# Performance work log

Hardware: AMD Instinct MI355X
Metric: run time of the kernel (lower is better)

Reference implementation:

```python
import jax, jax.numpy as jnp
import numpy as np

N_ATOMS = 5000
N_EDGES = 100000
F = 128          # num_features
B = 20           # num_basis (sinc expansion)
L = 3            # num_interactions
CUTOFF = 5.0
NUM_EMB = 119


def setup_inputs() -> dict:
    key = jax.random.key(0)
    ks = jax.random.split(key, 16)
    Z = jax.random.randint(ks[0], (N_ATOMS,), 1, NUM_EMB)
    edge_idx = jax.random.randint(ks[1], (N_EDGES, 2), 0, N_ATOMS)
    edge_dist = jax.random.uniform(ks[2], (N_EDGES,), minval=0.5, maxval=6.0, dtype=jnp.float32)
    u = jax.random.normal(ks[3], (N_EDGES, 3), dtype=jnp.float32)
    u = u / jnp.linalg.norm(u, axis=-1, keepdims=True)
    edge_diff = u * edge_dist[:, None]  # displacement vectors with |d| == edge_dist
    s = lambda k, shape: (jax.random.normal(k, shape, dtype=jnp.float32) * 0.05)
    inp = dict(Z=Z, edge_idx=edge_idx, edge_diff=edge_diff, edge_dist=edge_dist)
    inp.update(
        emb=s(ks[4], (NUM_EMB, F)),
        msg_w1=s(ks[5], (L, F, F)), msg_b1=jnp.zeros((L, F), jnp.float32),
        msg_w2=s(ks[6], (L, F, 3 * F)), msg_b2=jnp.zeros((L, 3 * F), jnp.float32),
        filt_w=s(ks[7], (L, B, 3 * F)), filt_b=jnp.zeros((L, 3 * F), jnp.float32),
        upd_U=s(ks[8], (L, F, F)), upd_V=s(ks[9], (L, F, F)),
        upd_w1=s(ks[10], (L, 2 * F, F)), upd_b1=jnp.zeros((L, F), jnp.float32),
        upd_w2=s(ks[11], (L, F, 3 * F)), upd_b2=jnp.zeros((L, 3 * F), jnp.float32),
        ro_w1=s(ks[12], (F, F // 2)), ro_b1=jnp.zeros((F // 2,), jnp.float32),
        ro_w2=s(ks[13], (F // 2, 1)), ro_b2=jnp.zeros((1,), jnp.float32),
    )
    return inp


def _painn(Z, edge_idx, edge_diff, edge_dist,
           emb, msg_w1, msg_b1, msg_w2, msg_b2, filt_w, filt_b,
           upd_U, upd_V, upd_w1, upd_b1, upd_w2, upd_b2,
           ro_w1, ro_b1, ro_w2, ro_b2):
    dtype = edge_diff.dtype
    # edge mask (equivalent to boolean compaction: masked edges contribute 0)
    mask = (edge_dist < CUTOFF).astype(dtype)
    dst = edge_idx[:, 0]  # receiver (index_add target)
    src = edge_idx[:, 1]  # sender (gathered neighbor)
    # sinc radial expansion: sin(n*pi*r/rc)/r, n = 1..B
    n = jnp.arange(1, B + 1, dtype=dtype)
    rbf = jnp.sin(edge_dist[:, None] * n * (jnp.pi / CUTOFF)) / edge_dist[:, None]  # [E,B]
    # cosine cutoff envelope, zeroed outside cutoff
    fc = 0.5 * (jnp.cos(jnp.pi * edge_dist / CUTOFF) + 1.0)
    env = (fc * mask)[:, None]  # [E,1]
    unit = edge_diff / edge_dist[:, None]  # [E,3]

    s_feat = emb[Z]                                   # [N,F]
    v_feat = jnp.zeros((Z.shape[0], 3, F), dtype)     # [N,3,F]

    for l in range(L):
        # ---- PainnMessage ----
        filt = (rbf @ filt_w[l] + filt_b[l]) * env                           # [E,3F]
        phi = jax.nn.silu(s_feat @ msg_w1[l] + msg_b1[l]) @ msg_w2[l] + msg_b2[l]  # [N,3F]
        fo = filt * phi[src]                                                  # [E,3F]
        gsv, gev, ms = jnp.split(fo, 3, axis=-1)                              # each [E,F]
        mv = v_feat[src] * gsv[:, None, :] + gev[:, None, :] * unit[:, :, None]  # [E,3,F]
        s_feat = s_feat + jnp.zeros_like(s_feat).at[dst].add(ms)
        v_feat = v_feat + jnp.zeros_like(v_feat).at[dst].add(mv)
        # ---- PainnUpdate ----
        Uv = jnp.einsum('nif,fg->nig', v_feat, upd_U[l])   # [N,3,F]
        Vv = jnp.einsum('nif,fg->nig', v_feat, upd_V[l])   # [N,3,F]
        Vn = jnp.linalg.norm(Vv, axis=1)                   # [N,F]
        a = jax.nn.silu(jnp.concatenate([s_feat, Vn], axis=-1) @ upd_w1[l] + upd_b1[l]) @ upd_w2[l] + upd_b2[l]
        avv, asv, ass = jnp.split(a, 3, axis=-1)
        v_feat = v_feat + avv[:, None, :] * Uv
        s_feat = s_feat + asv * jnp.sum(Uv * Vv, axis=1) + ass

    # atomwise readout MLP -> per-atom energy
    atom_energy = (jax.nn.silu(s_feat @ ro_w1 + ro_b1) @ ro_w2 + ro_b2)[:, 0]  # [N]
    return atom_energy


def reference(Z, edge_idx, edge_diff, edge_dist,
              emb, msg_w1, msg_b1, msg_w2, msg_b2, filt_w, filt_b,
              upd_U, upd_V, upd_w1, upd_b1, upd_w2, upd_b2,
              ro_w1, ro_b1, ro_w2, ro_b2):
    return _painn(Z, edge_idx, edge_diff, edge_dist,
                  emb, msg_w1, msg_b1, msg_w2, msg_b2, filt_w, filt_b,
                  upd_U, upd_V, upd_w1, upd_b1, upd_w2, upd_b2,
                  ro_w1, ro_b1, ro_w2, ro_b2)
```

## Files before the change

kernel.cpp:

```cpp
#include <hip/hip_runtime.h>
#include <hip/hip_bf16.h>
#include <hip/hip_fp16.h>
#include <math.h>

#define N_ATOMS 5000
#define N_EDGES 100000
#define F 128
#define B 20
#define NL 3
#define CAP 64

constexpr float CUTOFF = 5.0f;
constexpr float PI_F = 3.14159265358979323846f;

typedef _Float16 f16x8 __attribute__((ext_vector_type(8)));
typedef _Float16 h2 __attribute__((ext_vector_type(2)));
typedef float f32x4 __attribute__((ext_vector_type(4)));

struct EMeta { int src; float env; float u0, u1, u2; int pad[3]; };
struct __align__(4) U3 { unsigned int x, y, z; };

__device__ __forceinline__ float silu_f(float x) { return x / (1.0f + __expf(-x)); }

#define PV_IDX(atom, t) (((size_t)(atom) * F + (t)) * 6)

__global__ void init_kernel(const int* __restrict__ Z, const float* __restrict__ emb,
                            float* __restrict__ s, _Float16* __restrict__ s_h,
                            float* __restrict__ v, _Float16* __restrict__ pv,
                            int* __restrict__ count) {
    int atom = blockIdx.x;
    int t = threadIdx.x;
    float val = emb[Z[atom] * F + t];
    s[atom * F + t] = val;
    s_h[atom * F + t] = (_Float16)val;
#pragma unroll
    for (int d = 0; d < 3; ++d) v[(size_t)atom * 3 * F + d * F + t] = 0.0f;
    unsigned int* pp = (unsigned int*)(pv + PV_IDX(atom, t));
    pp[0] = 0u; pp[1] = 0u; pp[2] = 0u;
    if (t == 0) count[atom] = 0;
}

__global__ void fill_buckets(const int* __restrict__ eidx, int* __restrict__ count,
                             int* __restrict__ bucket) {
    int e = blockIdx.x * 256 + threadIdx.x;
    if (e >= N_EDGES) return;
    int dst = eidx[2 * e];
    int pos = atomicAdd(&count[dst], 1);
    if (pos < CAP) bucket[dst * CAP + pos] = e;
}

__global__ void edge_meta_kernel(const int* __restrict__ count, const int* __restrict__ bucket,
                                 const int* __restrict__ eidx, const float* __restrict__ ediff,
                                 const float* __restrict__ edist,
                                 EMeta* __restrict__ meta, _Float16* __restrict__ rbfh) {
    int slot = blockIdx.x * 256 + threadIdx.x;
    if (slot >= N_ATOMS * CAP) return;
    int a = slot / CAP, i = slot % CAP;
    if (i >= count[a]) return;
    int e = bucket[slot];
    float d = edist[e];
    EMeta m;
    m.src = eidx[2 * e + 1];
    float fc = 0.5f * (cosf(PI_F * d / CUTOFF) + 1.0f);
    m.env = (d < CUTOFF) ? fc : 0.0f;
    float inv = 1.0f / d;
    m.u0 = ediff[3 * e + 0] * inv;
    m.u1 = ediff[3 * e + 1] * inv;
    m.u2 = ediff[3 * e + 2] * inv;
    m.pad[0] = m.pad[1] = m.pad[2] = 0;
    meta[slot] = m;
    _Float16* rp = rbfh + (size_t)slot * 24;
#pragma unroll
    for (int b = 0; b < B; ++b)
        rp[b] = (_Float16)(sinf(d * (float)(b + 1) * (PI_F / CUTOFF)) / d);
    rp[20] = rp[21] = rp[22] = rp[23] = (_Float16)0.0f;
}

struct TPlanX { const float* src; void* dst; int R, C, blk0, isf16, pad; };
struct TPlansX { TPlanX p[24]; int n; };

__global__ void transpose_x(TPlansX P) {
    int b = blockIdx.x;
    int pi = 0;
#pragma unroll
    for (int i = 1; i < 24; ++i)
        if (i < P.n && b >= P.p[i].blk0) pi = i;
    const float* src = P.p[pi].src;
    int R = P.p[pi].R, C = P.p[pi].C, pad = P.p[pi].pad;
    int f = (b - P.p[pi].blk0) * 256 + threadIdx.x;
    if (f < R * C) {
        int c = f / R, r = f - c * R;
        float val = src[r * C + c];
        if (P.p[pi].isf16) ((_Float16*)P.p[pi].dst)[c * pad + r] = (_Float16)val;
        else ((float*)P.p[pi].dst)[c * pad + r] = val;
    }
}

__global__ __launch_bounds__(256) void phi_mlp_kernel(
    const _Float16* __restrict__ s_h, const _Float16* __restrict__ w1T,
    const float* __restrict__ b1, const _Float16* __restrict__ w2T,
    const float* __restrict__ b2, _Float16* __restrict__ pv) {
    __shared__ __align__(16) _Float16 shA[16 * 136];
    __shared__ __align__(16) _Float16 shH[16 * 136];
    int r0 = blockIdx.x * 16;
    int tid = threadIdx.x;
    {
        int r = tid >> 4, c8 = (tid & 15) * 8;
        int rg = r0 + r; if (rg >= N_ATOMS) rg = N_ATOMS - 1;
        *(f16x8*)(shA + r * 136 + c8) = *(const f16x8*)(s_h + (size_t)rg * F + c8);
    }
    __syncthreads();
    int lane = tid & 63, wv = tid >> 6;
    int col = lane & 15, quad = lane >> 4;
    for (int nt = wv; nt < 8; nt += 4) {
        int n = nt * 16 + col;
        f32x4 acc = {0.f, 0.f, 0.f, 0.f};
#pragma unroll
        for (int kt = 0; kt < 4; ++kt) {
            f16x8 afr = *(const f16x8*)(shA + col * 136 + kt * 32 + quad * 8);
            f16x8 bfr = *(const f16x8*)(w1T + (size_t)n * 128 + kt * 32 + quad * 8);
            acc = __builtin_amdgcn_mfma_f32_16x16x32_f16(afr, bfr, acc, 0, 0, 0);
        }
        float bb = b1[n];
#pragma unroll
        for (int r = 0; r < 4; ++r)
            shH[(quad * 4 + r) * 136 + n] = (_Float16)silu_f(acc[r] + bb);
    }
    __syncthreads();
    for (int nt = wv; nt < 24; nt += 4) {
        int n = nt * 16 + col;
        f32x4 acc = {0.f, 0.f, 0.f, 0.f};
#pragma unroll
        for (int kt = 0; kt < 4; ++kt) {
            f16x8 afr = *(const f16x8*)(shH + col * 136 + kt * 32 + quad * 8);
            f16x8 bfr = *(const f16x8*)(w2T + (size_t)n * 128 + kt * 32 + quad * 8);
            acc = __builtin_amdgcn_mfma_f32_16x16x32_f16(afr, bfr, acc, 0, 0, 0);
        }
        float bb = b2[n];
#pragma unroll
        for (int r = 0; r < 4; ++r) {
            int row = r0 + quad * 4 + r;
            if (row < N_ATOMS)
                pv[PV_IDX(row, n & 127) + (n >> 7)] = (_Float16)(acc[r] + bb);
        }
    }
}

__global__ __launch_bounds__(256) void edge_agg_kernel(
    const int* __restrict__ count, const EMeta* __restrict__ meta,
    const _Float16* __restrict__ rbfh,
    const _Float16* __restrict__ fwT,
    const float* __restrict__ fb,
    const _Float16* __restrict__ pv,
    float* __restrict__ s, float* __restrict__ v,
    _Float16* __restrict__ vmid_h) {
    int a = blockIdx.x;
    int tid = threadIdx.x;
    int t = tid & 127;
    int team = tid >> 7;

    unsigned int rw0[10], rw1[10], rw2[10];
    {
        const unsigned int* p0 = (const unsigned int*)(fwT + (size_t)t * 24);
        const unsigned int* p1 = (const unsigned int*)(fwT + (size_t)(F + t) * 24);
        const unsigned int* p2 = (const unsigned int*)(fwT + (size_t)(2 * F + t) * 24);
#pragma unroll
        for (int j = 0; j < 10; ++j) { rw0[j] = p0[j]; rw1[j] = p1[j]; rw2[j] = p2[j]; }
    }
    float fb0 = fb[t], fb1 = fb[F + t], fb2 = fb[2 * F + t];

    int n = count[a]; if (n > CAP) n = CAP;
    float accS = 0.f, accV0 = 0.f, accV1 = 0.f, accV2 = 0.f;

    __shared__ int sh_src[32];
    __shared__ float sh_env[32];
    __shared__ float sh_unit[32][3];
    __shared__ __align__(16) unsigned int sh_rbf[32 * 12];
    __shared__ __align__(16) float sh_part[4][F];
    const size_t aC = (size_t)a * CAP;
    const unsigned int* rbf32 = (const unsigned int*)rbfh;

    for (int base = 0; base < n; base += 32) {
        int cnt = min(32, n - base);
        __syncthreads();
        if (tid < cnt) {
            EMeta m = meta[aC + base + tid];
            sh_src[tid] = m.src;
            sh_env[tid] = m.env;
            sh_unit[tid][0] = m.u0; sh_unit[tid][1] = m.u1; sh_unit[tid][2] = m.u2;
        }
        for (int task = tid; task < cnt * 12; task += 256) {
            int i = task / 12, w = task - i * 12;
            sh_rbf[i * 12 + w] = rbf32[(aC + base + i) * 12 + w];
        }
        __syncthreads();

        int myCnt = (cnt > team) ? ((cnt - team + 1) >> 1) : 0;
        if (myCnt > 0) {
            U3 QA[4], QB[4];
            int ngrp = (myCnt + 3) >> 2;

            auto load_grp = [&](int gbase, U3 Q[4]) {
#pragma unroll
                for (int j = 0; j < 4; ++j) {
                    int i = gbase + j;
                    int ii = (i < myCnt) ? i : (myCnt - 1);
                    int src = sh_src[team + 2 * ii];
                    Q[j] = *(const U3*)(pv + PV_IDX(src, t));
                }
            };
            auto comp_grp = [&](int gbase, U3 Q[4]) {
#pragma unroll
                for (int j = 0; j < 4; ++j) {
                    int i = gbase + j;
                    if (i < myCnt) {
                        int ei = team + 2 * i;
                        const uint4* rq = (const uint4*)(sh_rbf + ei * 12);
                        uint4 qa = rq[0], qb = rq[1];
                        uint2 qc = *(const uint2*)(sh_rbf + ei * 12 + 8);
                        unsigned int rr[10] = {qa.x, qa.y, qa.z, qa.w,
                                               qb.x, qb.y, qb.z, qb.w, qc.x, qc.y};
                        float f0 = fb0, f1 = fb1, f2 = fb2;
#pragma unroll
                        for (int p = 0; p < 10; ++p) {
                            h2 rb = __builtin_bit_cast(h2, rr[p]);
                            f0 = __builtin_amdgcn_fdot2(rb, __builtin_bit_cast(h2, rw0[p]), f0, false);
                            f1 = __builtin_amdgcn_fdot2(rb, __builtin_bit_cast(h2, rw1[p]), f1, false);
                            f2 = __builtin_amdgcn_fdot2(rb, __builtin_bit_cast(h2, rw2[p]), f2, false);
                        }
                        float env = sh_env[ei];
                        f0 *= env; f1 *= env; f2 *= env;
                        h2 q0 = __builtin_bit_cast(h2, Q[j].x);
                        h2 q1 = __builtin_bit_cast(h2, Q[j].y);
                        h2 q2 = __builtin_bit_cast(h2, Q[j].z);
                        accS += f2 * (float)q1[0];
                        float gsv = f0 * (float)q0[0];
                        float gev = f1 * (float)q0[1];
                        accV0 += (float)q1[1] * gsv + gev * sh_unit[ei][0];
                        accV1 += (float)q2[0] * gsv + gev * sh_unit[ei][1];
                        accV2 += (float)q2[1] * gsv + gev * sh_unit[ei][2];
                    }
                }
            };

            load_grp(0, QA);
            for (int g = 0; g < ngrp; g += 2) {
                if (g + 1 < ngrp) load_grp((g + 1) * 4, QB);
                comp_grp(g * 4, QA);
                if (g + 1 < ngrp) {
                    if (g + 2 < ngrp) load_grp((g + 2) * 4, QA);
                    comp_grp((g + 1) * 4, QB);
                }
            }
        }
    }

    __syncthreads();
    if (team == 1) {
        sh_part[0][t] = accS; sh_part[1][t] = accV0;
        sh_part[2][t] = accV1; sh_part[3][t] = accV2;
    }
    __syncthreads();
    if (team == 0) {
        float sm = s[a * F + t] + accS + sh_part[0][t];
        s[a * F + t] = sm;
        float vm0 = v[a * 3 * F + t] + accV0 + sh_part[1][t];
        float vm1 = v[a * 3 * F + F + t] + accV1 + sh_part[2][t];
        float vm2 = v[a * 3 * F + 2 * F + t] + accV2 + sh_part[3][t];
        v[a * 3 * F + t] = vm0;
        v[a * 3 * F + F + t] = vm1;
        v[a * 3 * F + 2 * F + t] = vm2;
        vmid_h[(size_t)(a * 3 + 0) * F + t] = (_Float16)vm0;
        vmid_h[(size_t)(a * 3 + 1) * F + t] = (_Float16)vm1;
        vmid_h[(size_t)(a * 3 + 2) * F + t] = (_Float16)vm2;
    }
}

__global__ __launch_bounds__(512) void fused_update_kernel(
    const _Float16* __restrict__ vmid_h, const _Float16* __restrict__ uvT,
    const _Float16* __restrict__ w1T, const float* __restrict__ b1,
    const _Float16* __restrict__ w2T, const float* __restrict__ b2,
    float* __restrict__ s, float* __restrict__ v, _Float16* __restrict__ pv,
    const _Float16* __restrict__ nw1T, const float* __restrict__ nb1,
    const _Float16* __restrict__ nw2T, const float* __restrict__ nb2,
    int do_phi,
    const _Float16* __restrict__ roT16, const float* __restrict__ rb1,
    const float* __restrict__ rw2, const float* __restrict__ rb2,
    float* __restrict__ out, int do_ro) {
    __shared__ __align__(16) _Float16 shA[48 * 136];
    __shared__ __align__(16) _Float16 shUV[48 * 264];
    __shared__ __align__(16) _Float16 shCat[16 * 264];
    __shared__ __align__(16) _Float16 shH[16 * 136];
    __shared__ __align__(16) _Float16 shAa[16 * 392];
    _Float16* shS = shA;
    float* shRO = (float*)shAa;
    int a0 = blockIdx.x * 16;
    int r0 = a0 * 3;
    int tid = threadIdx.x;
    for (int slot = tid; slot < 48 * 16; slot += 512) {
        int r = slot >> 4, c8 = (slot & 15) * 8;
        int rg = r0 + r; if (rg >= N_ATOMS * 3) rg = N_ATOMS * 3 - 1;
        *(f16x8*)(shA + r * 136 + c8) = *(const f16x8*)(vmid_h + (size_t)rg * F + c8);
    }
    __syncthreads();
    int lane = tid & 63, wv = tid >> 6;
    int col = lane & 15, quad = lane >> 4;

    for (int j = wv; j < 48; j += 8) {
        int mt = j >> 4, nt = j & 15;
        int n = nt * 16 + col;
        f32x4 acc = {0.f, 0.f, 0.f, 0.f};
#pragma unroll
        for (int kt = 0; kt < 4; ++kt) {
            f16x8 afr = *(const f16x8*)(shA + (mt * 16 + col) * 136 + kt * 32 + quad * 8);
            f16x8 bfr = *(const f16x8*)(uvT + (size_t)n * 128 + kt * 32 + quad * 8);
            acc = __builtin_amdgcn_mfma_f32_16x16x32_f16(afr, bfr, acc, 0, 0, 0);
        }
#pragma unroll
        for (int r = 0; r < 4; ++r)
            shUV[(mt * 16 + quad * 4 + r) * 264 + n] = (_Float16)acc[r];
    }
    __syncthreads();

    for (int p = tid; p < 2048; p += 512) {
        int ai = p >> 7, t = p & 127;
        int atom = a0 + ai;
        int ag = (atom < N_ATOMS) ? atom : N_ATOMS - 1;
        shCat[ai * 264 + t] = (_Float16)s[(size_t)ag * F + t];
        float x0 = (float)shUV[(ai * 3 + 0) * 264 + 128 + t];
        float x1 = (float)shUV[(ai * 3 + 1) * 264 + 128 + t];
        float x2 = (float)shUV[(ai * 3 + 2) * 264 + 128 + t];
        shCat[ai * 264 + 128 + t] = (_Float16)sqrtf(x0 * x0 + x1 * x1 + x2 * x2);
    }
    __syncthreads();

    for (int nt = wv; nt < 8; nt += 8) {
        int n = nt * 16 + col;
        f32x4 acc = {0.f, 0.f, 0.f, 0.f};
#pragma unroll
        for (int kt = 0; kt < 8; ++kt) {
            f16x8 afr = *(const f16x8*)(shCat + col * 264 + kt * 32 + quad * 8);
            f16x8 bfr = *(const f16x8*)(w1T + (size_t)n * 256 + kt * 32 + quad * 8);
            acc = __builtin_amdgcn_mfma_f32_16x16x32_f16(afr, bfr, acc, 0, 0, 0);
        }
        float bb = b1[n];
#pragma unroll
        for (int r = 0; r < 4; ++r)
            shH[(quad * 4 + r) * 136 + n] = (_Float16)silu_f(acc[r] + bb);
    }
    __syncthreads();

    for (int nt = wv; nt < 24; nt += 8) {
        int n = nt * 16 + col;
        f32x4 acc = {0.f, 0.f, 0.f, 0.f};
#pragma unroll
        for (int kt = 0; kt < 4; ++kt) {
            f16x8 afr = *(const f16x8*)(shH + col * 136 + kt * 32 + quad * 8);
            f16x8 bfr = *(const f16x8*)(w2T + (size_t)n * 128 + kt * 32 + quad * 8);
            acc = __builtin_amdgcn_mfma_f32_16x16x32_f16(afr, bfr, acc, 0, 0, 0);
        }
        float bb = b2[n];
#pragma unroll
        for (int r = 0; r < 4; ++r)
            shAa[(quad * 4 + r) * 392 + n] = (_Float16)(acc[r] + bb);
    }
    __syncthreads();

    for (int p = tid; p < 2048; p += 512) {
        int ai = p >> 7, t = p & 127;
        int atom = a0 + ai;
        if (atom >= N_ATOMS) { shS[ai * 136 + t] = (_Float16)0.0f; continue; }
        float avv = (float)shAa[ai * 392 + t];
        float asv = (float)shAa[ai * 392 + 128 + t];
        float ass = (float)shAa[ai * 392 + 256 + t];
        float dot = 0.f;
        _Float16* pvp = pv + PV_IDX(atom, t);
#pragma unroll
        for (int d = 0; d < 3; ++d) {
            float u = (float)shUV[(ai * 3 + d) * 264 + t];
            float w = (float)shUV[(ai * 3 + d) * 264 + 128 + t];
            dot += u * w;
            float nv = v[(size_t)atom * 3 * F + d * F + t] + avv * u;
            v[(size_t)atom * 3 * F + d * F + t] = nv;
            pvp[3 + d] = (_Float16)nv;
        }
        float sn = s[(size_t)atom * F + t] + asv * dot + ass;
        s[(size_t)atom * F + t] = sn;
        shS[ai * 136 + t] = (_Float16)sn;
    }

    if (do_phi) {
        __syncthreads();
        for (int nt = wv; nt < 8; nt += 8) {
            int n = nt * 16 + col;
            f32x4 acc = {0.f, 0.f, 0.f, 0.f};
#pragma unroll
            for (int kt = 0; kt < 4; ++kt) {
                f16x8 afr = *(const f16x8*)(shS + col * 136 + kt * 32 + quad * 8);
                f16x8 bfr = *(const f16x8*)(nw1T + (size_t)n * 128 + kt * 32 + quad * 8);
                acc = __builtin_amdgcn_mfma_f32_16x16x32_f16(afr, bfr, acc, 0, 0, 0);
            }
            float bb = nb1[n];
#pragma unroll
            for (int r = 0; r < 4; ++r)
                shH[(quad * 4 + r) * 136 + n] = (_Float16)silu_f(acc[r] + bb);
        }
        __syncthreads();
        for (int nt = wv; nt < 24; nt += 8) {
            int n = nt * 16 + col;
            f32x4 acc = {0.f, 0.f, 0.f, 0.f};
#pragma unroll
            for (int kt = 0; kt < 4; ++kt) {
                f16x8 afr = *(const f16x8*)(shH + col * 136 + kt * 32 + quad * 8);
                f16x8 bfr = *(const f16x8*)(nw2T + (size_t)n * 128 + kt * 32 + quad * 8);
                acc = __builtin_amdgcn_mfma_f32_16x16x32_f16(afr, bfr, acc, 0, 0, 0);
            }
            float bb = nb2[n];
#pragma unroll
            for (int r = 0; r < 4; ++r) {
                int row = a0 + quad * 4 + r;
                if (row < N_ATOMS)
                    pv[PV_IDX(row, n & 127) + (n >> 7)] = (_Float16)(acc[r] + bb);
            }
        }
    }

    if (do_ro) {
        __syncthreads();
        if (wv < 4) {
            int n = wv * 16 + col;
            f32x4 acc = {0.f, 0.f, 0.f, 0.f};
#pragma unroll
            for (int kt = 0; kt < 4; ++kt) {
                f16x8 afr = *(const f16x8*)(shS + col * 136 + kt * 32 + quad * 8);
                f16x8 bfr = *(const f16x8*)(roT16 + (size_t)n * 128 + kt * 32 + quad * 8);
                acc = __builtin_amdgcn_mfma_f32_16x16x32_f16(afr, bfr, acc, 0, 0, 0);
            }
            float bb = rb1[n], w2n = rw2[n];
#pragma unroll
            for (int r = 0; r < 4; ++r)
                shRO[(quad * 4 + r) * 68 + n] = silu_f(acc[r] + bb) * w2n;
        }
        __syncthreads();
        if (tid < 16) {
            int atom = a0 + tid;
            if (atom < N_ATOMS) {
                float sum = rb2[0];
#pragma unroll 8
                for (int k = 0; k < 64; ++k) sum += shRO[tid * 68 + k];
                out[atom] = sum;
            }
        }
    }
}

extern "C" void kernel_launch(void* const* d_in, const int* in_sizes, int n_in,
                              void* d_out, int out_size, void* d_ws, size_t ws_size,
                              hipStream_t stream) {
    const int*   Z      = (const int*)d_in[0];
    const int*   eidx   = (const int*)d_in[1];
    const float* ediff  = (const float*)d_in[2];
    const float* edist  = (const float*)d_in[3];
    const float* emb    = (const float*)d_in[4];
    const float* msg_w1 = (const float*)d_in[5];
    const float* msg_b1 = (const float*)d_in[6];
    const float* msg_w2 = (const float*)d_in[7];
    const float* msg_b2 = (const float*)d_in[8];
    const float* filt_w = (const float*)d_in[9];
    const float* filt_b = (const float*)d_in[10];
    const float* upd_U  = (const float*)d_in[11];
    const float* upd_V  = (const float*)d_in[12];
    const float* upd_w1 = (const float*)d_in[13];
    const float* upd_b1 = (const float*)d_in[14];
    const float* upd_w2 = (const float*)d_in[15];
    const float* upd_b2 = (const float*)d_in[16];
    const float* ro_w1  = (const float*)d_in[17];
    const float* ro_b1  = (const float*)d_in[18];
    const float* ro_w2  = (const float*)d_in[19];
    const float* ro_b2  = (const float*)d_in[20];
    float* out = (float*)d_out;

    float* ws = (float*)d_ws;
    float* s   = ws;
    float* v   = s + N_ATOMS * F;
    int* count  = (int*)(v + N_ATOMS * 3 * F);
    int* bucket = count + N_ATOMS;
    EMeta* meta = (EMeta*)(bucket + N_ATOMS * CAP);
    _Float16* rbfh = (_Float16*)(meta + N_ATOMS * CAP);
    _Float16* s_h    = rbfh + (size_t)N_ATOMS * CAP * 24;
    _Float16* vmid_h = s_h + (size_t)N_ATOMS * F;
    _Float16* pv     = vmid_h + (size_t)N_ATOMS * 3 * F;
    _Float16* wh     = pv + (size_t)N_ATOMS * F * 6;

    const int HWL = 16384 + 49152 + 32768 + 32768 + 49152 + 384 * 24;
    _Float16* mw1T = wh;
    _Float16* mw2T = wh + 16384;
    _Float16* uvT  = wh + 65536;
    _Float16* uw1T = wh + 98304;
    _Float16* uw2T = wh + 131072;
    _Float16* fwTl = wh + 180224;
    _Float16* roT16 = wh + (size_t)NL * HWL;

    TPlansX P; int nb = 0, pi = 0;
    auto add = [&](const float* src, void* dst, int R, int C, int isf16, int pad) {
        P.p[pi].src = src; P.p[pi].dst = dst; P.p[pi].R = R; P.p[pi].C = C;
        P.p[pi].blk0 = nb; P.p[pi].isf16 = isf16; P.p[pi].pad = pad;
        nb += (R * C + 255) / 256; ++pi;
    };
    for (int l = 0; l < NL; ++l) {
        add(msg_w1 + l * F * F,     mw1T + (size_t)l * HWL, F, F, 1, F);
        add(msg_w2 + l * F * 3 * F, mw2T + (size_t)l * HWL, F, 3 * F, 1, F);
        add(upd_U  + l * F * F,     uvT  + (size_t)l * HWL, F, F, 1, F);
        add(upd_V  + l * F * F,     uvT  + (size_t)l * HWL + F * F, F, F, 1, F);
        add(upd_w1 + l * 2 * F * F, uw1T + (size_t)l * HWL, 2 * F, F, 1, 2 * F);
        add(upd_w2 + l * F * 3 * F, uw2T + (size_t)l * HWL, F, 3 * F, 1, F);
        add(filt_w + l * B * 3 * F, fwTl + (size_t)l * HWL, B, 3 * F, 1, 24);
    }
    add(ro_w1, roT16, F, 64, 1, F);
    P.n = pi;

    init_kernel<<<N_ATOMS, F, 0, stream>>>(Z, emb, s, s_h, v, pv, count);
    fill_buckets<<<(N_EDGES + 255) / 256, 256, 0, stream>>>(eidx, count, bucket);
    transpose_x<<<nb, 256, 0, stream>>>(P);
    edge_meta_kernel<<<(N_ATOMS * CAP + 255) / 256, 256, 0, stream>>>(
        count, bucket, eidx, ediff, edist, meta, rbfh);

    const int GB16 = (N_ATOMS + 15) / 16;
    phi_mlp_kernel<<<GB16, 256, 0, stream>>>(
        s_h, mw1T, msg_b1, mw2T, msg_b2, pv);
    for (int l = 0; l < NL; ++l) {
        edge_agg_kernel<<<N_ATOMS, 256, 0, stream>>>(
            count, meta, rbfh, fwTl + (size_t)l * HWL, filt_b + l * 3 * F,
            pv, s, v, vmid_h);
        int do_phi = (l + 1 < NL);
        int do_ro = (l == NL - 1);
        int ln = do_phi ? (l + 1) : l;
        fused_update_kernel<<<GB16, 512, 0, stream>>>(
            vmid_h, uvT + (size_t)l * HWL,
            uw1T + (size_t)l * HWL, upd_b1 + l * F,
            uw2T + (size_t)l * HWL, upd_b2 + l * 3 * F,
            s, v, pv,
            mw1T + (size_t)ln * HWL, msg_b1 + ln * F,
            mw2T + (size_t)ln * HWL, msg_b2 + ln * 3 * F, do_phi,
            roT16, ro_b1, ro_w2, ro_b2, out, do_ro);
    }
}
```

Measured before the change: 359.3 us.

## Fuse edge aggregation with node update per layer and merge setup kernels

Merges the per-layer edge aggregation and update kernels into one layer kernel that handles 16 atoms per block. Edge metadata and rbf are staged in shared memory, and the aggregated s/v stay in registers instead of round-tripping through vmid_h. The pv buffer is double-buffered (ping-pong) so the next layer's phi output can be written while neighbours still read the old one. Setup work (init, bucket fill, tiled weight transpose) is combined into one kernel, and edge-meta is combined with the first phi MLP, to cut launch count. The cost is lower block parallelism in the edge phase (313 blocks instead of 5000) and heavy shared-memory use per block, which limits occupancy.

```diff
diff --git a/kernel.cpp b/kernel.cpp
--- a/kernel.cpp
+++ b/kernel.cpp
@@ -24,86 +24,103 @@
 
 #define PV_IDX(atom, t) (((size_t)(atom) * F + (t)) * 6)
 
-__global__ void init_kernel(const int* __restrict__ Z, const float* __restrict__ emb,
-                            float* __restrict__ s, _Float16* __restrict__ s_h,
-                            float* __restrict__ v, _Float16* __restrict__ pv,
-                            int* __restrict__ count) {
-    int atom = blockIdx.x;
-    int t = threadIdx.x;
-    float val = emb[Z[atom] * F + t];
-    s[atom * F + t] = val;
-    s_h[atom * F + t] = (_Float16)val;
-#pragma unroll
-    for (int d = 0; d < 3; ++d) v[(size_t)atom * 3 * F + d * F + t] = 0.0f;
-    unsigned int* pp = (unsigned int*)(pv + PV_IDX(atom, t));
-    pp[0] = 0u; pp[1] = 0u; pp[2] = 0u;
-    if (t == 0) count[atom] = 0;
+#define NB_INIT 2500
+#define NB_BUCK 391
+
+struct TPlanT { const float* src; _Float16* dst; int R, C, pad, blk0, tpc; };
+struct TPlansT { TPlanT p[22]; int n; };
+
+__global__ __launch_bounds__(256) void prep_kernel(
+    const int* __restrict__ Z, const float* __restrict__ emb,
+    float* __restrict__ s, _Float16* __restrict__ s_h,
+    float* __restrict__ v, _Float16* __restrict__ pv,
+    const int* __restrict__ eidx, int* __restrict__ count, int* __restrict__ bucket,
+    TPlansT P) {
+    __shared__ float tile[32][33];
+    int b = blockIdx.x, tid = threadIdx.x;
+    if (b < NB_INIT) {
+        int atom = b * 2 + (tid >> 7);
+        int t = tid & 127;
+        float val = emb[Z[atom] * F + t];
+        s[(size_t)atom * F + t] = val;
+        s_h[(size_t)atom * F + t] = (_Float16)val;
+#pragma unroll
+        for (int d = 0; d < 3; ++d) v[((size_t)atom * 3 + d) * F + t] = 0.0f;
+        unsigned int* pp = (unsigned int*)(pv + PV_IDX(atom, t));
+        pp[0] = 0u; pp[1] = 0u; pp[2] = 0u;
+        return;
+    }
+    if (b < NB_INIT + NB_BUCK) {
+        int e = (b - NB_INIT) * 256 + tid;
+        if (e < N_EDGES) {
+            int dst = eidx[2 * e];
+            int pos = atomicAdd(&count[dst], 1);
+            if (pos < CAP) bucket[dst * CAP + pos] = e;
+        }
+        return;
+    }
+    int tb = b - (NB_INIT + NB_BUCK);
+    int pi = 0;
+#pragma unroll
+    for (int i = 1; i < 22; ++i)
+        if (i < P.n && tb >= P.p[i].blk0) pi = i;
+    const float* src = P.p[pi].src;
+    _Float16* dst = P.p[pi].dst;
+    int R = P.p[pi].R, C = P.p[pi].C, pad = P.p[pi].pad;
+    int tl = tb - P.p[pi].blk0;
+    int tpc = P.p[pi].tpc;
+    int tr0 = (tl / tpc) * 32, tc0 = (tl % tpc) * 32;
+    int i = tid >> 5, j = tid & 31;
+#pragma unroll
+    for (int rr = 0; rr < 4; ++rr) {
+        int r = tr0 + i + 8 * rr, c = tc0 + j;
+        if (r < R && c < C) tile[i + 8 * rr][j] = src[(size_t)r * C + c];
+    }
+    __syncthreads();
+#pragma unroll
+    for (int rr = 0; rr < 4; ++rr) {
+        int c = tc0 + i + 8 * rr, r = tr0 + j;
+        if (c < C && r < R) dst[(size_t)c * pad + r] = (_Float16)tile[j][i + 8 * rr];
+    }
 }
 
-__global__ void fill_buckets(const int* __restrict__ eidx, int* __restrict__ count,
-                             int* __restrict__ bucket) {
-    int e = blockIdx.x * 256 + threadIdx.x;
-    if (e >= N_EDGES) return;
-    int dst = eidx[2 * e];
-    int pos = atomicAdd(&count[dst], 1);
-    if (pos < CAP) bucket[dst * CAP + pos] = e;
-}
-
-__global__ void edge_meta_kernel(const int* __restrict__ count, const int* __restrict__ bucket,
-                                 const int* __restrict__ eidx, const float* __restrict__ ediff,
-                                 const float* __restrict__ edist,
-                                 EMeta* __restrict__ meta, _Float16* __restrict__ rbfh) {
-    int slot = blockIdx.x * 256 + threadIdx.x;
-    if (slot >= N_ATOMS * CAP) return;
-    int a = slot / CAP, i = slot % CAP;
-    if (i >= count[a]) return;
-    int e = bucket[slot];
-    float d = edist[e];
-    EMeta m;
-    m.src = eidx[2 * e + 1];
-    float fc = 0.5f * (cosf(PI_F * d / CUTOFF) + 1.0f);
-    m.env = (d < CUTOFF) ? fc : 0.0f;
-    float inv = 1.0f / d;
-    m.u0 = ediff[3 * e + 0] * inv;
-    m.u1 = ediff[3 * e + 1] * inv;
-    m.u2 = ediff[3 * e + 2] * inv;
-    m.pad[0] = m.pad[1] = m.pad[2] = 0;
-    meta[slot] = m;
-    _Float16* rp = rbfh + (size_t)slot * 24;
-#pragma unroll
-    for (int b = 0; b < B; ++b)
-        rp[b] = (_Float16)(sinf(d * (float)(b + 1) * (PI_F / CUTOFF)) / d);
-    rp[20] = rp[21] = rp[22] = rp[23] = (_Float16)0.0f;
-}
-
-struct TPlanX { const float* src; void* dst; int R, C, blk0, isf16, pad; };
-struct TPlansX { TPlanX p[24]; int n; };
-
-__global__ void transpose_x(TPlansX P) {
-    int b = blockIdx.x;
-    int pi = 0;
-#pragma unroll
-    for (int i = 1; i < 24; ++i)
-        if (i < P.n && b >= P.p[i].blk0) pi = i;
-    const float* src = P.p[pi].src;
-    int R = P.p[pi].R, C = P.p[pi].C, pad = P.p[pi].pad;
-    int f = (b - P.p[pi].blk0) * 256 + threadIdx.x;
-    if (f < R * C) {
-        int c = f / R, r = f - c * R;
-        float val = src[r * C + c];
-        if (P.p[pi].isf16) ((_Float16*)P.p[pi].dst)[c * pad + r] = (_Float16)val;
-        else ((float*)P.p[pi].dst)[c * pad + r] = val;
-    }
-}
-
-__global__ __launch_bounds__(256) void phi_mlp_kernel(
+#define NB_META 1250
+
+__global__ __launch_bounds__(256) void meta_phi_kernel(
+    const int* __restrict__ count, const int* __restrict__ bucket,
+    const int* __restrict__ eidx, const float* __restrict__ ediff,
+    const float* __restrict__ edist,
+    EMeta* __restrict__ meta, _Float16* __restrict__ rbfh,
     const _Float16* __restrict__ s_h, const _Float16* __restrict__ w1T,
     const float* __restrict__ b1, const _Float16* __restrict__ w2T,
     const float* __restrict__ b2, _Float16* __restrict__ pv) {
     __shared__ __align__(16) _Float16 shA[16 * 136];
     __shared__ __align__(16) _Float16 shH[16 * 136];
-    int r0 = blockIdx.x * 16;
-    int tid = threadIdx.x;
+    int b = blockIdx.x, tid = threadIdx.x;
+    if (b < NB_META) {
+        int slot = b * 256 + tid;
+        int a = slot >> 6, i = slot & (CAP - 1);
+        if (i >= count[a]) return;
+        int e = bucket[slot];
+        float d = edist[e];
+        EMeta m;
+        m.src = eidx[2 * e + 1];
+        float fc = 0.5f * (cosf(PI_F * d / CUTOFF) + 1.0f);
+        m.env = (d < CUTOFF) ? fc : 0.0f;
+        float inv = 1.0f / d;
+        m.u0 = ediff[3 * e + 0] * inv;
+        m.u1 = ediff[3 * e + 1] * inv;
+        m.u2 = ediff[3 * e + 2] * inv;
+        m.pad[0] = m.pad[1] = m.pad[2] = 0;
+        meta[slot] = m;
+        _Float16* rp = rbfh + (size_t)slot * 24;
+#pragma unroll
+        for (int bb = 0; bb < B; ++bb)
+            rp[bb] = (_Float16)(sinf(d * (float)(bb + 1) * (PI_F / CUTOFF)) / d);
+        rp[20] = rp[21] = rp[22] = rp[23] = (_Float16)0.0f;
+        return;
+    }
+    int r0 = (b - NB_META) * 16;
     {
         int r = tid >> 4, c8 = (tid & 15) * 8;
         int rg = r0 + r; if (rg >= N_ATOMS) rg = N_ATOMS - 1;
@@ -146,165 +163,153 @@
     }
 }
 
-__global__ __launch_bounds__(256) void edge_agg_kernel(
+__global__ __launch_bounds__(512, 4) void layer_kernel(
     const int* __restrict__ count, const EMeta* __restrict__ meta,
     const _Float16* __restrict__ rbfh,
-    const _Float16* __restrict__ fwT,
-    const float* __restrict__ fb,
-    const _Float16* __restrict__ pv,
+    const _Float16* __restrict__ fwT, const float* __restrict__ fb,
+    const _Float16* __restrict__ uvT,
+    const _Float16* __restrict__ w1T, const float* __restrict__ b1,
+    const _Float16* __restrict__ w2T, const float* __restrict__ b2,
     float* __restrict__ s, float* __restrict__ v,
-    _Float16* __restrict__ vmid_h) {
-    int a = blockIdx.x;
+    const _Float16* __restrict__ pv_r, _Float16* __restrict__ pv_w,
+    const _Float16* __restrict__ nw1T, const float* __restrict__ nb1,
+    const _Float16* __restrict__ nw2T, const float* __restrict__ nb2, int do_phi,
+    const _Float16* __restrict__ roT16, const float* __restrict__ rb1,
+    const float* __restrict__ ro_w2p, const float* __restrict__ rb2,
+    float* __restrict__ out, int do_ro) {
+    __shared__ __align__(16) _Float16 shV16[48 * 136];
+    __shared__ __align__(16) unsigned char shU[61440];
+    int* sh_src           = (int*)shU;
+    float* sh_env         = (float*)(shU + 4096);
+    float* sh_unit        = (float*)(shU + 8192);
+    unsigned int* sh_rbfA = (unsigned int*)(shU + 20480);
+    unsigned int* sh_rbfB = (unsigned int*)(shU + 53248);
+    _Float16* shUV  = (_Float16*)shU;
+    _Float16* shCat = (_Float16*)(shU + 25344);
+    _Float16* shH   = (_Float16*)(shU + 33792);
+    _Float16* shAa  = (_Float16*)(shU + 38144);
+    float* shRO     = (float*)(shU + 38144);
+    _Float16* shS16 = shV16;
+
+    int a0 = blockIdx.x * 16;
     int tid = threadIdx.x;
-    int t = tid & 127;
-    int team = tid >> 7;
-
-    unsigned int rw0[10], rw1[10], rw2[10];
+    int t = tid & 127, team = tid >> 7;
+    int lane = tid & 63, wv = tid >> 6;
+    int col = lane & 15, quad = lane >> 4;
+
+    unsigned int frw0[10], frw1[10], frw2[10];
     {
         const unsigned int* p0 = (const unsigned int*)(fwT + (size_t)t * 24);
         const unsigned int* p1 = (const unsigned int*)(fwT + (size_t)(F + t) * 24);
         const unsigned int* p2 = (const unsigned int*)(fwT + (size_t)(2 * F + t) * 24);
 #pragma unroll
-        for (int j = 0; j < 10; ++j) { rw0[j] = p0[j]; rw1[j] = p1[j]; rw2[j] = p2[j]; }
+        for (int j = 0; j < 10; ++j) { frw0[j] = p0[j]; frw1[j] = p1[j]; frw2[j] = p2[j]; }
     }
     float fb0 = fb[t], fb1 = fb[F + t], fb2 = fb[2 * F + t];
 
-    int n = count[a]; if (n > CAP) n = CAP;
-    float accS = 0.f, accV0 = 0.f, accV1 = 0.f, accV2 = 0.f;
-
-    __shared__ int sh_src[32];
-    __shared__ float sh_env[32];
-    __shared__ float sh_unit[32][3];
-    __shared__ __align__(16) unsigned int sh_rbf[32 * 12];
-    __shared__ __align__(16) float sh_part[4][F];
-    const size_t aC = (size_t)a * CAP;
-    const unsigned int* rbf32 = (const unsigned int*)rbfh;
-
-    for (int base = 0; base < n; base += 32) {
-        int cnt = min(32, n - base);
-        __syncthreads();
-        if (tid < cnt) {
-            EMeta m = meta[aC + base + tid];
-            sh_src[tid] = m.src;
-            sh_env[tid] = m.env;
-            sh_unit[tid][0] = m.u0; sh_unit[tid][1] = m.u1; sh_unit[tid][2] = m.u2;
-        }
-        for (int task = tid; task < cnt * 12; task += 256) {
-            int i = task / 12, w = task - i * 12;
-            sh_rbf[i * 12 + w] = rbf32[(aC + base + i) * 12 + w];
-        }
-        __syncthreads();
-
-        int myCnt = (cnt > team) ? ((cnt - team + 1) >> 1) : 0;
-        if (myCnt > 0) {
-            U3 QA[4], QB[4];
-            int ngrp = (myCnt + 3) >> 2;
-
-            auto load_grp = [&](int gbase, U3 Q[4]) {
-#pragma unroll
-                for (int j = 0; j < 4; ++j) {
-                    int i = gbase + j;
-                    int ii = (i < myCnt) ? i : (myCnt - 1);
-                    int src = sh_src[team + 2 * ii];
-                    Q[j] = *(const U3*)(pv + PV_IDX(src, t));
-                }
-            };
-            auto comp_grp = [&](int gbase, U3 Q[4]) {
-#pragma unroll
-                for (int j = 0; j < 4; ++j) {
-                    int i = gbase + j;
-                    if (i < myCnt) {
-                        int ei = team + 2 * i;
-                        const uint4* rq = (const uint4*)(sh_rbf + ei * 12);
-                        uint4 qa = rq[0], qb = rq[1];
-                        uint2 qc = *(const uint2*)(sh_rbf + ei * 12 + 8);
-                        unsigned int rr[10] = {qa.x, qa.y, qa.z, qa.w,
-                                               qb.x, qb.y, qb.z, qb.w, qc.x, qc.y};
-                        float f0 = fb0, f1 = fb1, f2 = fb2;
-#pragma unroll
-                        for (int p = 0; p < 10; ++p) {
-                            h2 rb = __builtin_bit_cast(h2, rr[p]);
-                            f0 = __builtin_amdgcn_fdot2(rb, __builtin_bit_cast(h2, rw0[p]), f0, false);
-                            f1 = __builtin_amdgcn_fdot2(rb, __builtin_bit_cast(h2, rw1[p]), f1, false);
-                            f2 = __builtin_amdgcn_fdot2(rb, __builtin_bit_cast(h2, rw2[p]), f2, false);
+    for (int slot = tid; slot < 16 * CAP; slot += 512) {
+        int ai = slot >> 6;
+        int a = a0 + ai;
+        if (a < N_ATOMS) {
+            int i = slot & (CAP - 1);
+            int n = count[a]; if (n > CAP) n = CAP;
+            if (i < n) {
+                const EMeta m = meta[(size_t)a * CAP + i];
+                sh_src[slot] = m.src;
+                sh_env[slot] = m.env;
+                sh_unit[slot * 3 + 0] = m.u0;
+                sh_unit[slot * 3 + 1] = m.u1;
+                sh_unit[slot * 3 + 2] = m.u2;
+                const unsigned int* rp = (const unsigned int*)(rbfh + ((size_t)a * CAP + i) * 24);
+#pragma unroll
+                for (int j = 0; j < 8; ++j) sh_rbfA[slot * 8 + j] = rp[j];
+                sh_rbfB[slot * 2 + 0] = rp[8];
+                sh_rbfB[slot * 2 + 1] = rp[9];
+            }
+        }
+    }
+    __syncthreads();
+
+    float sR[4], vmR0[4], vmR1[4], vmR2[4];
+
+#pragma unroll
+    for (int g = 0; g < 4; ++g) {
+        int ai = team + 4 * g;
+        int a = a0 + ai;
+        float accS = 0.f, accV0 = 0.f, accV1 = 0.f, accV2 = 0.f;
+        float s_old = 0.f, v_old0 = 0.f, v_old1 = 0.f, v_old2 = 0.f;
+        if (a < N_ATOMS) {
+            s_old = s[(size_t)a * F + t];
+            v_old0 = v[((size_t)a * 3 + 0) * F + t];
+            v_old1 = v[((size_t)a * 3 + 1) * F + t];
+            v_old2 = v[((size_t)a * 3 + 2) * F + t];
+            int n = count[a]; if (n > CAP) n = CAP;
+            if (n > 0) {
+                const int base = ai * CAP;
+                U3 QA[4], QB[4];
+                int ngrp = (n + 3) >> 2;
+                auto load_grp = [&](int gb, U3 Q[4]) {
+#pragma unroll
+                    for (int j = 0; j < 4; ++j) {
+                        int i = gb + j;
+                        int ii = (i < n) ? i : (n - 1);
+                        int sidx = sh_src[base + ii];
+                        Q[j] = *(const U3*)(pv_r + PV_IDX(sidx, t));
+                    }
+                };
+                auto comp_grp = [&](int gb, U3 Q[4]) {
+#pragma unroll
+                    for (int j = 0; j < 4; ++j) {
+                        int i = gb + j;
+                        if (i < n) {
+                            int ei = base + i;
+                            uint4 qa = *(const uint4*)(sh_rbfA + ei * 8);
+                            uint4 qb = *(const uint4*)(sh_rbfA + ei * 8 + 4);
+                            uint2 qc = *(const uint2*)(sh_rbfB + ei * 2);
+                            unsigned int rr[10] = {qa.x, qa.y, qa.z, qa.w,
+                                                   qb.x, qb.y, qb.z, qb.w, qc.x, qc.y};
+                            float f0 = fb0, f1 = fb1, f2 = fb2;
+#pragma unroll
+                            for (int p = 0; p < 10; ++p) {
+                                h2 rb = __builtin_bit_cast(h2, rr[p]);
+                                f0 = __builtin_amdgcn_fdot2(rb, __builtin_bit_cast(h2, frw0[p]), f0, false);
+                                f1 = __builtin_amdgcn_fdot2(rb, __builtin_bit_cast(h2, frw1[p]), f1, false);
+                                f2 = __builtin_amdgcn_fdot2(rb, __builtin_bit_cast(h2, frw2[p]), f2, false);
+                            }
+                            float env = sh_env[ei];
+                            f0 *= env; f1 *= env; f2 *= env;
+                            h2 q0 = __builtin_bit_cast(h2, Q[j].x);
+                            h2 q1 = __builtin_bit_cast(h2, Q[j].y);
+                            h2 q2 = __builtin_bit_cast(h2, Q[j].z);
+                            accS += f2 * (float)q1[0];
+                            float gsv = f0 * (float)q0[0];
+                            float gev = f1 * (float)q0[1];
+                            accV0 += (float)q1[1] * gsv + gev * sh_unit[ei * 3 + 0];
+                            accV1 += (float)q2[0] * gsv + gev * sh_unit[ei * 3 + 1];
+                            accV2 += (float)q2[1] * gsv + gev * sh_unit[ei * 3 + 2];
                         }
-                        float env = sh_env[ei];
-                        f0 *= env; f1 *= env; f2 *= env;
-                        h2 q0 = __builtin_bit_cast(h2, Q[j].x);
-                        h2 q1 = __builtin_bit_cast(h2, Q[j].y);
-                        h2 q2 = __builtin_bit_cast(h2, Q[j].z);
-                        accS += f2 * (float)q1[0];
-                        float gsv = f0 * (float)q0[0];
-                        float gev = f1 * (float)q0[1];
-                        accV0 += (float)q1[1] * gsv + gev * sh_unit[ei][0];
-                        accV1 += (float)q2[0] * gsv + gev * sh_unit[ei][1];
-                        accV2 += (float)q2[1] * gsv + gev * sh_unit[ei][2];
+                    }
+                };
+                load_grp(0, QA);
+                for (int gg = 0; gg < ngrp; gg += 2) {
+                    if (gg + 1 < ngrp) load_grp((gg + 1) * 4, QB);
+                    comp_grp(gg * 4, QA);
+                    if (gg + 1 < ngrp) {
+                        if (gg + 2 < ngrp) load_grp((gg + 2) * 4, QA);
+                        comp_grp((gg + 1) * 4, QB);
                     }
                 }
-            };
-
-            load_grp(0, QA);
-            for (int g = 0; g < ngrp; g += 2) {
-                if (g + 1 < ngrp) load_grp((g + 1) * 4, QB);
-                comp_grp(g * 4, QA);
-                if (g + 1 < ngrp) {
-                    if (g + 2 < ngrp) load_grp((g + 2) * 4, QA);
-                    comp_grp((g + 1) * 4, QB);
-                }
-            }
-        }
-    }
-
-    __syncthreads();
-    if (team == 1) {
-        sh_part[0][t] = accS; sh_part[1][t] = accV0;
-        sh_part[2][t] = accV1; sh_part[3][t] = accV2;
-    }
-    __syncthreads();
-    if (team == 0) {
-        float sm = s[a * F + t] + accS + sh_part[0][t];
-        s[a * F + t] = sm;
-        float vm0 = v[a * 3 * F + t] + accV0 + sh_part[1][t];
-        float vm1 = v[a * 3 * F + F + t] + accV1 + sh_part[2][t];
-        float vm2 = v[a * 3 * F + 2 * F + t] + accV2 + sh_part[3][t];
-        v[a * 3 * F + t] = vm0;
-        v[a * 3 * F + F + t] = vm1;
-        v[a * 3 * F + 2 * F + t] = vm2;
-        vmid_h[(size_t)(a * 3 + 0) * F + t] = (_Float16)vm0;
-        vmid_h[(size_t)(a * 3 + 1) * F + t] = (_Float16)vm1;
-        vmid_h[(size_t)(a * 3 + 2) * F + t] = (_Float16)vm2;
-    }
-}
-
-__global__ __launch_bounds__(512) void fused_update_kernel(
-    const _Float16* __restrict__ vmid_h, const _Float16* __restrict__ uvT,
-    const _Float16* __restrict__ w1T, const float* __restrict__ b1,
-    const _Float16* __restrict__ w2T, const float* __restrict__ b2,
-    float* __restrict__ s, float* __restrict__ v, _Float16* __restrict__ pv,
-    const _Float16* __restrict__ nw1T, const float* __restrict__ nb1,
-    const _Float16* __restrict__ nw2T, const float* __restrict__ nb2,
-    int do_phi,
-    const _Float16* __restrict__ roT16, const float* __restrict__ rb1,
-    const float* __restrict__ rw2, const float* __restrict__ rb2,
-    float* __restrict__ out, int do_ro) {
-    __shared__ __align__(16) _Float16 shA[48 * 136];
-    __shared__ __align__(16) _Float16 shUV[48 * 264];
-    __shared__ __align__(16) _Float16 shCat[16 * 264];
-    __shared__ __align__(16) _Float16 shH[16 * 136];
-    __shared__ __align__(16) _Float16 shAa[16 * 392];
-    _Float16* shS = shA;
-    float* shRO = (float*)shAa;
-    int a0 = blockIdx.x * 16;
-    int r0 = a0 * 3;
-    int tid = threadIdx.x;
-    for (int slot = tid; slot < 48 * 16; slot += 512) {
-        int r = slot >> 4, c8 = (slot & 15) * 8;
-        int rg = r0 + r; if (rg >= N_ATOMS * 3) rg = N_ATOMS * 3 - 1;
-        *(f16x8*)(shA + r * 136 + c8) = *(const f16x8*)(vmid_h + (size_t)rg * F + c8);
-    }
-    __syncthreads();
-    int lane = tid & 63, wv = tid >> 6;
-    int col = lane & 15, quad = lane >> 4;
+            }
+        }
+        sR[g] = s_old + accS;
+        vmR0[g] = v_old0 + accV0;
+        vmR1[g] = v_old1 + accV1;
+        vmR2[g] = v_old2 + accV2;
+        shV16[(ai * 3 + 0) * 136 + t] = (_Float16)vmR0[g];
+        shV16[(ai * 3 + 1) * 136 + t] = (_Float16)vmR1[g];
+        shV16[(ai * 3 + 2) * 136 + t] = (_Float16)vmR2[g];
+    }
+    __syncthreads();
 
     for (int j = wv; j < 48; j += 8) {
         int mt = j >> 4, nt = j & 15;
@@ -312,7 +317,7 @@
         f32x4 acc = {0.f, 0.f, 0.f, 0.f};
 #pragma unroll
         for (int kt = 0; kt < 4; ++kt) {
-            f16x8 afr = *(const f16x8*)(shA + (mt * 16 + col) * 136 + kt * 32 + quad * 8);
+            f16x8 afr = *(const f16x8*)(shV16 + (mt * 16 + col) * 136 + kt * 32 + quad * 8);
             f16x8 bfr = *(const f16x8*)(uvT + (size_t)n * 128 + kt * 32 + quad * 8);
             acc = __builtin_amdgcn_mfma_f32_16x16x32_f16(afr, bfr, acc, 0, 0, 0);
         }
@@ -322,11 +327,10 @@
     }
     __syncthreads();
 
-    for (int p = tid; p < 2048; p += 512) {
-        int ai = p >> 7, t = p & 127;
-        int atom = a0 + ai;
-        int ag = (atom < N_ATOMS) ? atom : N_ATOMS - 1;
-        shCat[ai * 264 + t] = (_Float16)s[(size_t)ag * F + t];
+#pragma unroll
+    for (int g = 0; g < 4; ++g) {
+        int ai = team + 4 * g;
+        shCat[ai * 264 + t] = (_Float16)sR[g];
         float x0 = (float)shUV[(ai * 3 + 0) * 264 + 128 + t];
         float x1 = (float)shUV[(ai * 3 + 1) * 264 + 128 + t];
         float x2 = (float)shUV[(ai * 3 + 2) * 264 + 128 + t];
@@ -366,27 +370,34 @@
     }
     __syncthreads();
 
-    for (int p = tid; p < 2048; p += 512) {
-        int ai = p >> 7, t = p & 127;
+#pragma unroll
+    for (int g = 0; g < 4; ++g) {
+        int ai = team + 4 * g;
         int atom = a0 + ai;
-        if (atom >= N_ATOMS) { shS[ai * 136 + t] = (_Float16)0.0f; continue; }
+        if (atom >= N_ATOMS) { shS16[ai * 136 + t] = (_Float16)0.0f; continue; }
         float avv = (float)shAa[ai * 392 + t];
         float asv = (float)shAa[ai * 392 + 128 + t];
         float ass = (float)shAa[ai * 392 + 256 + t];
-        float dot = 0.f;
-        _Float16* pvp = pv + PV_IDX(atom, t);
-#pragma unroll
-        for (int d = 0; d < 3; ++d) {
-            float u = (float)shUV[(ai * 3 + d) * 264 + t];
-            float w = (float)shUV[(ai * 3 + d) * 264 + 128 + t];
-            dot += u * w;
-            float nv = v[(size_t)atom * 3 * F + d * F + t] + avv * u;
-            v[(size_t)atom * 3 * F + d * F + t] = nv;
-            pvp[3 + d] = (_Float16)nv;
-        }
-        float sn = s[(size_t)atom * F + t] + asv * dot + ass;
+        _Float16* pvp = pv_w + PV_IDX(atom, t);
+        float u0_ = (float)shUV[(ai * 3 + 0) * 264 + t];
+        float w0_ = (float)shUV[(ai * 3 + 0) * 264 + 128 + t];
+        float u1_ = (float)shUV[(ai * 3 + 1) * 264 + t];
+        float w1_ = (float)shUV[(ai * 3 + 1) * 264 + 128 + t];
+        float u2_ = (float)shUV[(ai * 3 + 2) * 264 + t];
+        float w2_ = (float)shUV[(ai * 3 + 2) * 264 + 128 + t];
+        float dot = u0_ * w0_ + u1_ * w1_ + u2_ * w2_;
+        float nv0 = vmR0[g] + avv * u0_;
+        float nv1 = vmR1[g] + avv * u1_;
+        float nv2 = vmR2[g] + avv * u2_;
+        v[((size_t)atom * 3 + 0) * F + t] = nv0;
+        v[((size_t)atom * 3 + 1) * F + t] = nv1;
+        v[((size_t)atom * 3 + 2) * F + t] = nv2;
+        pvp[3] = (_Float16)nv0;
+        pvp[4] = (_Float16)nv1;
+        pvp[5] = (_Float16)nv2;
+        float sn = sR[g] + asv * dot + ass;
         s[(size_t)atom * F + t] = sn;
-        shS[ai * 136 + t] = (_Float16)sn;
+        shS16[ai * 136 + t] = (_Float16)sn;
     }
 
     if (do_phi) {
@@ -396,7 +407,7 @@
             f32x4 acc = {0.f, 0.f, 0.f, 0.f};
 #pragma unroll
             for (int kt = 0; kt < 4; ++kt) {
-                f16x8 afr = *(const f16x8*)(shS + col * 136 + kt * 32 + quad * 8);
+                f16x8 afr = *(const f16x8*)(shS16 + col * 136 + kt * 32 + quad * 8);
                 f16x8 bfr = *(const f16x8*)(nw1T + (size_t)n * 128 + kt * 32 + quad * 8);
                 acc = __builtin_amdgcn_mfma_f32_16x16x32_f16(afr, bfr, acc, 0, 0, 0);
             }
@@ -420,7 +431,7 @@
             for (int r = 0; r < 4; ++r) {
                 int row = a0 + quad * 4 + r;
                 if (row < N_ATOMS)
-                    pv[PV_IDX(row, n & 127) + (n >> 7)] = (_Float16)(acc[r] + bb);
+                    pv_w[PV_IDX(row, n & 127) + (n >> 7)] = (_Float16)(acc[r] + bb);
             }
         }
     }
@@ -432,11 +443,11 @@
             f32x4 acc = {0.f, 0.f, 0.f, 0.f};
 #pragma unroll
             for (int kt = 0; kt < 4; ++kt) {
-                f16x8 afr = *(const f16x8*)(shS + col * 136 + kt * 32 + quad * 8);
+                f16x8 afr = *(const f16x8*)(shS16 + col * 136 + kt * 32 + quad * 8);
                 f16x8 bfr = *(const f16x8*)(roT16 + (size_t)n * 128 + kt * 32 + quad * 8);
                 acc = __builtin_amdgcn_mfma_f32_16x16x32_f16(afr, bfr, acc, 0, 0, 0);
             }
-            float bb = rb1[n], w2n = rw2[n];
+            float bb = rb1[n], w2n = ro_w2p[n];
 #pragma unroll
             for (int r = 0; r < 4; ++r)
                 shRO[(quad * 4 + r) * 68 + n] = silu_f(acc[r] + bb) * w2n;
@@ -487,10 +498,10 @@
     int* bucket = count + N_ATOMS;
     EMeta* meta = (EMeta*)(bucket + N_ATOMS * CAP);
     _Float16* rbfh = (_Float16*)(meta + N_ATOMS * CAP);
-    _Float16* s_h    = rbfh + (size_t)N_ATOMS * CAP * 24;
-    _Float16* vmid_h = s_h + (size_t)N_ATOMS * F;
-    _Float16* pv     = vmid_h + (size_t)N_ATOMS * 3 * F;
-    _Float16* wh     = pv + (size_t)N_ATOMS * F * 6;
+    _Float16* s_h  = rbfh + (size_t)N_ATOMS * CAP * 24;
+    _Float16* pvA  = s_h + (size_t)N_ATOMS * F;
+    _Float16* pvB  = pvA + (size_t)N_ATOMS * F * 6;
+    _Float16* wh   = pvB + (size_t)N_ATOMS * F * 6;
 
     const int HWL = 16384 + 49152 + 32768 + 32768 + 49152 + 384 * 24;
     _Float16* mw1T = wh;
@@ -501,47 +512,52 @@
     _Float16* fwTl = wh + 180224;
     _Float16* roT16 = wh + (size_t)NL * HWL;
 
-    TPlansX P; int nb = 0, pi = 0;
-    auto add = [&](const float* src, void* dst, int R, int C, int isf16, int pad) {
-        P.p[pi].src = src; P.p[pi].dst = dst; P.p[pi].R = R; P.p[pi].C = C;
-        P.p[pi].blk0 = nb; P.p[pi].isf16 = isf16; P.p[pi].pad = pad;
-        nb += (R * C + 255) / 256; ++pi;
+    TPlansT P; int nb = 0, pi = 0;
+    auto add = [&](const float* src, _Float16* dst, int R, int C, int pad) {
+        int tr = (R + 31) / 32, tc = (C + 31) / 32;
+        P.p[pi].src = src; P.p[pi].dst = dst;
+        P.p[pi].R = R; P.p[pi].C = C; P.p[pi].pad = pad;
+        P.p[pi].blk0 = nb; P.p[pi].tpc = tc;
+        nb += tr * tc; ++pi;
     };
     for (int l = 0; l < NL; ++l) {
-        add(msg_w1 + l * F * F,     mw1T + (size_t)l * HWL, F, F, 1, F);
-        add(msg_w2 + l * F * 3 * F, mw2T + (size_t)l * HWL, F, 3 * F, 1, F);
-        add(upd_U  + l * F * F,     uvT  + (size_t)l * HWL, F, F, 1, F);
-        add(upd_V  + l * F * F,     uvT  + (size_t)l * HWL + F * F, F, F, 1, F);
-        add(upd_w1 + l * 2 * F * F, uw1T + (size_t)l * HWL, 2 * F, F, 1, 2 * F);
-        add(upd_w2 + l * F * 3 * F, uw2T + (size_t)l * HWL, F, 3 * F, 1, F);
-        add(filt_w + l * B * 3 * F, fwTl + (size_t)l * HWL, B, 3 * F, 1, 24);
-    }
-    add(ro_w1, roT16, F, 64, 1, F);
+        add(msg_w1 + l * F * F,     mw1T + (size_t)l * HWL, F, F, F);
+        add(msg_w2 + l * F * 3 * F, mw2T + (size_t)l * HWL, F, 3 * F, F);
+        add(upd_U  + l * F * F,     uvT  + (size_t)l * HWL, F, F, F);
+        add(upd_V  + l * F * F,     uvT  + (size_t)l * HWL + F * F, F, F, F);
+        add(upd_w1 + l * 2 * F * F, uw1T + (size_t)l * HWL, 2 * F, F, 2 * F);
+        add(upd_w2 + l * F * 3 * F, uw2T + (size_t)l * HWL, F, 3 * F, F);
+        add(filt_w + l * B * 3 * F, fwTl + (size_t)l * HWL, B, 3 * F, 24);
+    }
+    add(ro_w1, roT16, F, 64, F);
     P.n = pi;
 
-    init_kernel<<<N_ATOMS, F, 0, stream>>>(Z, emb, s, s_h, v, pv, count);
-    fill_buckets<<<(N_EDGES + 255) / 256, 256, 0, stream>>>(eidx, count, bucket);
-    transpose_x<<<nb, 256, 0, stream>>>(P);
-    edge_meta_kernel<<<(N_ATOMS * CAP + 255) / 256, 256, 0, stream>>>(
-        count, bucket, eidx, ediff, edist, meta, rbfh);
+    (void)hipMemsetAsync(count, 0, N_ATOMS * sizeof(int), stream);
+
+    prep_kernel<<<NB_INIT + NB_BUCK + nb, 256, 0, stream>>>(
+        Z, emb, s, s_h, v, pvA, eidx, count, bucket, P);
 
     const int GB16 = (N_ATOMS + 15) / 16;
-    phi_mlp_kernel<<<GB16, 256, 0, stream>>>(
-        s_h, mw1T, msg_b1, mw2T, msg_b2, pv);
+    meta_phi_kernel<<<NB_META + GB16, 256, 0, stream>>>(
+        count, bucket, eidx, ediff, edist, meta, rbfh,
+        s_h, mw1T, msg_b1, mw2T, msg_b2, pvA);
+
+    _Float16* pr = pvA;
+    _Float16* pw = pvB;
     for (int l = 0; l < NL; ++l) {
-        edge_agg_kernel<<<N_ATOMS, 256, 0, stream>>>(
-            count, meta, rbfh, fwTl + (size_t)l * HWL, filt_b + l * 3 * F,
-            pv, s, v, vmid_h);
         int do_phi = (l + 1 < NL);
         int do_ro = (l == NL - 1);
         int ln = do_phi ? (l + 1) : l;
-        fused_update_kernel<<<GB16, 512, 0, stream>>>(
-            vmid_h, uvT + (size_t)l * HWL,
+        layer_kernel<<<GB16, 512, 0, stream>>>(
+            count, meta, rbfh,
+            fwTl + (size_t)l * HWL, filt_b + l * 3 * F,
+            uvT + (size_t)l * HWL,
             uw1T + (size_t)l * HWL, upd_b1 + l * F,
             uw2T + (size_t)l * HWL, upd_b2 + l * 3 * F,
-            s, v, pv,
+            s, v, pr, pw,
             mw1T + (size_t)ln * HWL, msg_b1 + ln * F,
             mw2T + (size_t)ln * HWL, msg_b2 + ln * 3 * F, do_phi,
             roT16, ro_b1, ro_w2, ro_b2, out, do_ro);
+        _Float16* tmp = pr; pr = pw; pw = tmp;
     }
 }
```

Result: no change. 355.7 us (-1.0%).
